# Performance work log

Hardware: AMD Instinct MI355X
Metric: run time of the kernel (lower is better)

## Reference

```python
import jax, jax.numpy as jnp
import numpy as np

ROPE_THETA = 10000.0

def _rope(t):
    # t: (B, S, H, D) -- rotate-half RoPE over last dim
    B, S, H, D = t.shape
    inv_freq = 1.0 / (ROPE_THETA ** (jnp.arange(0, D, 2, dtype=jnp.float32) / D))  # (D/2,)
    ang = jnp.arange(S, dtype=jnp.float32)[:, None] * inv_freq[None, :]            # (S, D/2)
    cos = jnp.concatenate([jnp.cos(ang), jnp.cos(ang)], axis=-1)[None, :, None, :] # (1,S,1,D)
    sin = jnp.concatenate([jnp.sin(ang), jnp.sin(ang)], axis=-1)[None, :, None, :]
    t1, t2 = jnp.split(t, 2, axis=-1)
    rot = jnp.concatenate([-t2, t1], axis=-1)
    return t * cos.astype(t.dtype) + rot * sin.astype(t.dtype)

def setup_inputs() -> dict:
    key = jax.random.key(0)
    kx, kq, kk, kv, ko = jax.random.split(key, 5)
    B, S, DIM = 2, 2048, 2048
    x = jax.random.normal(kx, (B, S, DIM), dtype=jnp.float32)
    mask = jnp.tril(jnp.ones((S, S), dtype=bool))[None, None, :, :]  # causal (1,1,S,S)
    scale = DIM ** -0.5
    wq = jax.random.normal(kq, (DIM, DIM), dtype=jnp.float32) * scale
    wk = jax.random.normal(kk, (DIM, DIM), dtype=jnp.float32) * scale
    wv = jax.random.normal(kv, (DIM, DIM), dtype=jnp.float32) * scale
    wo = jax.random.normal(ko, (DIM, DIM), dtype=jnp.float32) * scale
    return {"x": x, "mask": mask, "wq": wq, "wk": wk, "wv": wv, "wo": wo}

def reference(x, mask, wq, wk, wv, wo):
    B, S, DIM = x.shape
    H = 16
    D = DIM // H
    scale = D ** -0.5
    # nn.Linear: y = x @ W.T
    q = (x @ wq.T).reshape(B, S, H, D)
    k = (x @ wk.T).reshape(B, S, H, D)
    v = (x @ wv.T).reshape(B, S, H, D)
    q = _rope(q)
    k = _rope(k)
    scores = jnp.einsum('bqhd,bkhd->bhqk', q, k) * scale
    scores = jnp.where(mask, scores, -jnp.inf)
    attn = jax.nn.softmax(scores, axis=-1)
    out = jnp.einsum('bhqk,bkhd->bqhd', attn, v).reshape(B, S, DIM)
    return out @ wo.T
```

## Files before the change

### kernel.cpp

```cpp
#include <hip/hip_runtime.h>
#include <cstdint>

typedef unsigned short u16;
typedef uint32_t u32;
typedef __attribute__((ext_vector_type(8))) short bf16x8;
typedef __attribute__((ext_vector_type(4))) float f32x4;
typedef __attribute__((ext_vector_type(16))) float f32x16;

#define DIM_ 2048
#define S_   2048
#define B_   2
#define H_   16
#define HD_  128
#define M_   (B_ * S_)

__device__ __forceinline__ u16 f2b(float f) {
  union { float f; uint32_t u; } v; v.f = f;
  uint32_t u = v.u;
  return (u16)((u + 0x7FFFu + ((u >> 16) & 1u)) >> 16);
}
__device__ __forceinline__ float b2f(u16 h) {
  union { uint32_t u; float f; } v; v.u = ((uint32_t)h) << 16;
  return v.f;
}

__device__ __forceinline__ u32 cvtpk(float lo, float hi) {
  u32 r;
  asm("v_cvt_pk_bf16_f32 %0, %1, %2" : "=v"(r) : "v"(lo), "v"(hi));
  return r;
}

typedef __attribute__((address_space(3))) u16 lds_u16_t;
typedef __attribute__((address_space(1))) const u16 glob_u16_t;

__device__ __forceinline__ void gload16(const u16* g, u16* l) {
  __builtin_amdgcn_global_load_lds((glob_u16_t*)g, (lds_u16_t*)l, 16, 0, 0);
}
#define GLD0(SRC, DST) \
  __builtin_amdgcn_global_load_lds((glob_u16_t*)(SRC), (lds_u16_t*)(DST), 16, 0, 0)

__global__ void convert5_kernel(const float* __restrict__ x, const float* __restrict__ wq,
                                const float* __restrict__ wk, const float* __restrict__ wv,
                                const float* __restrict__ wo, u16* __restrict__ xb,
                                u16* __restrict__ wqb, u16* __restrict__ wkb,
                                u16* __restrict__ wvb, u16* __restrict__ wob) {
  const float* src;
  u16* dst;
  int n;
  switch (blockIdx.y) {
    case 0: src = x;  dst = xb;  n = M_ * DIM_;   break;
    case 1: src = wq; dst = wqb; n = DIM_ * DIM_; break;
    case 2: src = wk; dst = wkb; n = DIM_ * DIM_; break;
    case 3: src = wv; dst = wvb; n = DIM_ * DIM_; break;
    default: src = wo; dst = wob; n = DIM_ * DIM_; break;
  }
  int i = (blockIdx.x * blockDim.x + threadIdx.x) * 4;
  const int stride = gridDim.x * blockDim.x * 4;
  for (; i < n; i += stride) {
    float4 v = *reinterpret_cast<const float4*>(src + i);
    uint64_t p = (uint64_t)f2b(v.x) | ((uint64_t)f2b(v.y) << 16) |
                 ((uint64_t)f2b(v.z) << 32) | ((uint64_t)f2b(v.w) << 48);
    *reinterpret_cast<uint64_t*>(dst + i) = p;
  }
}

__global__ void rope_table_kernel(float* __restrict__ cosT, float* __restrict__ sinT) {
  int i = blockIdx.x * blockDim.x + threadIdx.x;
  if (i >= S_ * 64) return;
  int s = i >> 6, d = i & 63;
  float inv = powf(10000.0f, -(float)d * (1.0f / 64.0f));
  float ang = (float)s * inv;
  cosT[i] = cosf(ang);
  sinT[i] = sinf(ang);
}

#define NT_ 32

#define LDA(DST, BASE)                                                         \
  _Pragma("unroll") for (int mi = 0; mi < 8; ++mi)                             \
      DST[mi] = *(const bf16x8*)((BASE) + mi * 1024);
#define LDB(DST, BASE)                                                         \
  _Pragma("unroll") for (int ni = 0; ni < NF_; ++ni)                           \
      DST[ni] = *(const bf16x8*)((BASE) +                                      \
          (BPERM_ ? (((ni) & 1) * 1024 + ((ni) >> 1) * 4096) : (ni) * 1024));

#define MFMA_KS(AV, BV)                                                        \
  _Pragma("unroll") for (int mi = 0; mi < 8; ++mi)                             \
    _Pragma("unroll") for (int ni = 0; ni < NF_; ++ni)                         \
        acc[mi][ni] = __builtin_amdgcn_mfma_f32_16x16x32_bf16(                 \
            AV[mi], BV[ni], acc[mi][ni], 0, 0, 0);

#define STAGE(BUF, OFFU) do {                                                  \
    _Pragma("unroll") for (int s = 0; s < ASW_; ++s)                           \
      GLD0(sA + goff + (OFFU) + s * (64 * DIM_),                               \
           lds + (BUF) * BUFSZ_ + s * 4096 + w * 512);                         \
    _Pragma("unroll") for (int s = 0; s < BSW_; ++s)                           \
      GLD0(sB + goff + (OFFU) + s * (64 * DIM_),                               \
           lds + (BUF) * BUFSZ_ + 16384 + s * 4096 + w * 512);                 \
  } while (0)

#define VMC_N() do {                                                           \
    if (ASW_ + BSW_ == 8) asm volatile("s_waitcnt vmcnt(8)" ::: "memory");     \
    else                  asm volatile("s_waitcnt vmcnt(6)" ::: "memory");     \
  } while (0)

#define TILE_N(BUF, NBUF, OFFU) do {                                           \
    LDA(a1, pAk1[BUF]); LDB(b1, pBk1[BUF]);                            \
    __builtin_amdgcn_sched_barrier(0);                                         \
    __builtin_amdgcn_s_setprio(1);                                             \
    MFMA_KS(a0, b0);                                                  \
    __builtin_amdgcn_s_setprio(0);                                             \
    asm volatile("s_waitcnt lgkmcnt(0)" ::: "memory");                         \
    __builtin_amdgcn_sched_barrier(0);                                         \
    __builtin_amdgcn_s_barrier();                                      \
    STAGE(BUF, OFFU);                                                          \
    __builtin_amdgcn_sched_barrier(0);                                         \
    VMC_N();                                                                   \
    __builtin_amdgcn_sched_barrier(0);                                         \
    __builtin_amdgcn_s_barrier();                                      \
    LDA(a0, pAk0[NBUF]); LDB(b0, pBk0[NBUF]);                          \
    __builtin_amdgcn_sched_barrier(0);                                         \
    __builtin_amdgcn_s_setprio(1);                                             \
    MFMA_KS(a1, b1);                                                  \
    __builtin_amdgcn_s_setprio(0);                                             \
  } while (0)

#define TILE_P(BUF, NBUF) do {                                   \
    LDA(a1, pAk1[BUF]); LDB(b1, pBk1[BUF]);                                    \
    __builtin_amdgcn_sched_barrier(0);                                         \
    __builtin_amdgcn_s_setprio(1);                                             \
    MFMA_KS(a0, b0);                                                           \
    __builtin_amdgcn_s_setprio(0);                                             \
    asm volatile("s_waitcnt lgkmcnt(0)" ::: "memory");                         \
    __builtin_amdgcn_sched_barrier(0);                                         \
    asm volatile("s_waitcnt vmcnt(0)" ::: "memory");                           \
    __builtin_amdgcn_sched_barrier(0);                                         \
    __builtin_amdgcn_s_barrier();                                              \
    LDA(a0, pAk0[NBUF]); LDB(b0, pBk0[NBUF]);                                  \
    __builtin_amdgcn_sched_barrier(0);                                         \
    __builtin_amdgcn_s_setprio(1);                                             \
    MFMA_KS(a1, b1);                                                           \
    __builtin_amdgcn_s_setprio(0);                                             \
  } while (0)

#define TILE_L(BUF) do {                                         \
    LDA(a1, pAk1[BUF]); LDB(b1, pBk1[BUF]);                                    \
    __builtin_amdgcn_sched_barrier(0);                                         \
    MFMA_KS(a0, b0);                                                           \
    MFMA_KS(a1, b1);                                                           \
  } while (0)

#define GEMM_V2_BODY(BN_, BPERM__)                                             \
  constexpr int NF_ = (BN_) / 64;                                              \
  constexpr int BPERM_ = (BPERM__);                                            \
  constexpr int ASW_ = 4;                                                      \
  constexpr int BSW_ = (BN_) / 64;                                             \
  constexpr int BUFSZ_ = 16384 + (BN_) * 64;                                   \
  const int tid = threadIdx.x;                                                 \
  const int lane = tid & 63;                                                   \
  const int w = tid >> 6;                                                      \
  const int wm = w >> 2, wn = w & 3;                                           \
  const int l15 = lane & 15, lg = lane >> 4;                                   \
  const int goff = (w * 8 + (lane >> 3)) * DIM_ + ((lane & 7) ^ (lane >> 3)) * 8; \
  const int x7 = l15 & 7;                                                      \
  const int lr0 = l15 * 64 + ((lg ^ x7) * 8);                                  \
  const int lr1 = l15 * 64 + (((4 | lg) ^ x7) * 8);                            \
  const int bbase = BPERM_ ? ((wn >> 1) * 8192 + (wn & 1) * 2048)              \
                           : (wn * ((BN_) * 16));                              \
  const u16* pAk0[2] = {lds + wm * 8192 + lr0, lds + BUFSZ_ + wm * 8192 + lr0};\
  const u16* pAk1[2] = {lds + wm * 8192 + lr1, lds + BUFSZ_ + wm * 8192 + lr1};\
  const u16* pBk0[2] = {lds + 16384 + bbase + lr0,                             \
                        lds + BUFSZ_ + 16384 + bbase + lr0};                   \
  const u16* pBk1[2] = {lds + 16384 + bbase + lr1,                             \
                        lds + BUFSZ_ + 16384 + bbase + lr1};                   \
  f32x4 acc[8][NF_];                                                           \
  _Pragma("unroll") for (int i = 0; i < 8; ++i)                                \
    _Pragma("unroll") for (int j = 0; j < NF_; ++j)                            \
        acc[i][j] = (f32x4){0.f, 0.f, 0.f, 0.f};                               \
  bf16x8 a0[8], a1[8], b0[NF_], b1[NF_];                                       \
  STAGE(0, 0);                                                                 \
  STAGE(1, 64);                                                                \
  __builtin_amdgcn_sched_barrier(0);                                           \
  VMC_N();                                                                     \
  __builtin_amdgcn_sched_barrier(0);                                           \
  __builtin_amdgcn_s_barrier();                                                \
  LDA(a0, pAk0[0]); LDB(b0, pBk0[0]);                                          \
  for (int t = 0; t < NT_ - 2; t += 2) {                                       \
    TILE_N(0, 1, 128);                                                         \
    TILE_N(1, 0, 192);                                                         \
    sA += 128; sB += 128;                                                      \
  }                                                                            \
  TILE_P(0, 1);                                                                \
  TILE_L(1);

__global__ __launch_bounds__(512, 2) void gemm256_qkv_kernel(
    const u16* __restrict__ xb, const u16* __restrict__ wqb, const u16* __restrict__ wkb,
    const u16* __restrict__ wvb, u16* __restrict__ qb, u16* __restrict__ kb,
    u16* __restrict__ vb, const float* __restrict__ cosT, const float* __restrict__ sinT) {
  __shared__ __align__(16) u16 lds[65536];

  const int bid = blockIdx.x;
  const int logical = (bid & 7) * 48 + (bid >> 3);
  const int mt = logical / 24;
  const int rem = logical % 24;
  const int z = rem >> 3;
  const int nt = rem & 7;
  const u16* Wm = (z == 0) ? wqb : (z == 1) ? wkb : wvb;
  u16* out = (z == 0) ? qb : (z == 1) ? kb : vb;

  const u16* sA = xb + (size_t)(mt * 256) * DIM_;
  const u16* sB = Wm + (size_t)(nt * 256) * DIM_;

  GEMM_V2_BODY(256, 1)

  const int colbase = nt * 256 + (wn >> 1) * 128 + (wn & 1) * 32;
  if (z < 2) {
#pragma unroll
    for (int mi = 0; mi < 8; ++mi) {
      const int row = mt * 256 + wm * 128 + mi * 16 + lg * 4;
#pragma unroll
      for (int r = 0; r < 4; ++r) {
        const int s = (row + r) & (S_ - 1);
#pragma unroll
        for (int ni = 0; ni < 2; ++ni) {
          const int d = (wn & 1) * 32 + ni * 16 + l15;
          const float c  = cosT[s * 64 + d];
          const float sn = sinT[s * 64 + d];
          const float t1 = acc[mi][ni][r];
          const float t2 = acc[mi][ni + 2][r];
          u16* p = out + (size_t)(row + r) * DIM_ + colbase + ni * 16 + l15;
          p[0]  = f2b(t1 * c - t2 * sn);
          p[64] = f2b(t2 * c + t1 * sn);
        }
      }
    }
  } else {
#pragma unroll
    for (int mi = 0; mi < 8; ++mi)
#pragma unroll
      for (int ni = 0; ni < 4; ++ni) {
        const int row = mt * 256 + wm * 128 + mi * 16 + lg * 4;
        const int col = colbase + (ni & 1) * 16 + (ni >> 1) * 64 + l15;
#pragma unroll
        for (int r = 0; r < 4; ++r)
          out[(size_t)(row + r) * DIM_ + col] = f2b(acc[mi][ni][r]);
      }
  }
}

__global__ __launch_bounds__(512, 2) void gemm_out_v2_kernel(const u16* __restrict__ A,
                                                             const u16* __restrict__ W,
                                                             float* __restrict__ Cf) {
  __shared__ __align__(16) u16 lds[49152];
  const int bid = blockIdx.x;
  const int logical = (bid & 7) * 32 + (bid >> 3);
  const int mt = logical >> 4;
  const int nt = logical & 15;

  const u16* sA = A + (size_t)(mt * 256) * DIM_;
  const u16* sB = W + (size_t)(nt * 128) * DIM_;

  GEMM_V2_BODY(128, 0)

#pragma unroll
  for (int mi = 0; mi < 8; ++mi)
#pragma unroll
    for (int ni = 0; ni < 2; ++ni) {
      const int row = mt * 256 + wm * 128 + mi * 16 + lg * 4;
      const int col = nt * 128 + wn * 32 + ni * 16 + l15;
#pragma unroll
      for (int r = 0; r < 4; ++r)
        Cf[(size_t)(row + r) * DIM_ + col] = acc[mi][ni][r];
    }
}

#define CEXP 0.12751744f

__global__ __launch_bounds__(256, 2) void attn_kernel(const u16* __restrict__ q,
                                                      const u16* __restrict__ k,
                                                      const u16* __restrict__ v,
                                                      u16* __restrict__ ao) {
  __shared__ __align__(16) u16 smem[32768];
  u16* kTl = smem;
  u16* vTl = smem + 16384;

  const int r_    = blockIdx.x;
  const int qt   = 15 - (r_ >> 1);
  const int b    = r_ & 1;
  const int head = blockIdx.y;
  const int t = threadIdx.x;
  const int lane = t & 63;
  const int w = t >> 6;
  const int l31 = lane & 31;
  const int hi = lane >> 5;
  const int kxor = (lane & 7) << 3;
  const int qrow0 = qt * 128 + w * 32;
  const size_t bS = (size_t)b * S_;

  bf16x8 qf[8];
  {
    const u16* qrow = q + (bS + qrow0 + l31) * DIM_ + head * HD_;
#pragma unroll
    for (int st = 0; st < 8; ++st)
      qf[st] = *(const bf16x8*)(qrow + st * 16 + hi * 8);
  }

  f32x16 accO[4];
#pragma unroll
  for (int db = 0; db < 4; ++db)
#pragma unroll
    for (int rr = 0; rr < 16; ++rr) accO[db][rr] = 0.f;
  float m = -1e30f, l = 0.f;

  const int tmax_w = 2 * qt + (w >> 1);
  const int ttend = 2 * qt + 1;

  bf16x8 vv[4];

  auto stageK = [&](int buf, int tt) {
#pragma unroll
    for (int p = 0; p < 4; ++p) {
      const int cid = p * 256 + w * 64 + lane;
      const int kr = cid >> 4;
      const int cg = (cid & 15) ^ (kr & 7);
      gload16(k + (bS + tt * 64 + kr) * DIM_ + head * HD_ + cg * 8,
              kTl + buf * 8192 + (p * 256 + w * 64) * 8);
    }
  };
  auto loadV = [&](int tt) {
#pragma unroll
    for (int p = 0; p < 4; ++p) {
      const int dchunk = p * 4 + w;
      vv[p] = *(const bf16x8*)(v + (bS + tt * 64 + lane) * DIM_ + head * HD_ + dchunk * 8);
    }
  };
  auto writeV = [&](int buf) {
#pragma unroll
    for (int p = 0; p < 4; ++p) {
      const int dchunk = p * 4 + w;
#pragma unroll
      for (int j = 0; j < 8; ++j) {
        const int d = dchunk * 8 + j;
        vTl[buf * 8192 + d * 64 + (lane ^ ((d & 7) << 3))] = (u16)vv[p][j];
      }
    }
  };

  stageK(0, 0);
  loadV(0);
  writeV(0);
  __syncthreads();

  for (int tt = 0; tt <= ttend; ++tt) {
    const int cur = tt & 1;
    const int alt = cur ^ 1;

    if (tt + 1 <= ttend) {
      stageK(alt, tt + 1);
      loadV(tt + 1);
    }

    if (tt <= tmax_w) {
      const u16* kB = kTl + cur * 8192;
      const u16* vB = vTl + cur * 8192;
      f32x16 sA, sB;
#pragma unroll
      for (int rr = 0; rr < 16; ++rr) { sA[rr] = 0.f; sB[rr] = 0.f; }
      __builtin_amdgcn_s_setprio(1);
#pragma unroll
      for (int st = 0; st < 8; ++st) {
        const int dc = st * 16 + hi * 8;
        bf16x8 k0 = *(const bf16x8*)(kB + l31 * 128 + (dc ^ kxor));
        bf16x8 k1 = *(const bf16x8*)(kB + (32 + l31) * 128 + (dc ^ kxor));
        sA = __builtin_amdgcn_mfma_f32_32x32x16_bf16(k0, qf[st], sA, 0, 0, 0);
        sB = __builtin_amdgcn_mfma_f32_32x32x16_bf16(k1, qf[st], sB, 0, 0, 0);
      }
      __builtin_amdgcn_s_setprio(0);

      const int qg = qrow0 + l31;
      if (tt * 64 + 63 > qrow0) {
        const int kb = tt * 64 + 4 * hi;
#pragma unroll
        for (int rr = 0; rr < 16; ++rr) {
          const int kg = kb + (rr & 3) + 8 * (rr >> 2);
          sA[rr] = (kg <= qg) ? sA[rr] : -1e30f;
          sB[rr] = (kg + 32 <= qg) ? sB[rr] : -1e30f;
        }
      }

      float mx[8];
#pragma unroll
      for (int i = 0; i < 8; ++i)
        mx[i] = fmaxf(fmaxf(sA[i], sA[i + 8]), fmaxf(sB[i], sB[i + 8]));
#pragma unroll
      for (int i = 0; i < 4; ++i) mx[i] = fmaxf(mx[i], mx[i + 4]);
      float pm = fmaxf(fmaxf(mx[0], mx[1]), fmaxf(mx[2], mx[3]));
      pm = fmaxf(pm, __shfl_xor(pm, 32));
      const float mN = fmaxf(m, pm);
      if (!__all(pm - m <= 90.5f)) {
        const float osc = exp2f((m - mN) * CEXP);
        l *= osc;
#pragma unroll
        for (int db = 0; db < 4; ++db)
#pragma unroll
          for (int rr = 0; rr < 16; ++rr) accO[db][rr] *= osc;
        m = mN;
      }
      const float mc = m * CEXP;
      float lsv[4] = {0.f, 0.f, 0.f, 0.f};
#pragma unroll
      for (int rr = 0; rr < 16; ++rr) {
        const float pa = exp2f(__builtin_fmaf(sA[rr], CEXP, -mc));
        const float pb = exp2f(__builtin_fmaf(sB[rr], CEXP, -mc));
        sA[rr] = pa; sB[rr] = pb;
        lsv[rr & 3] += pa + pb;
      }
      float ls = (lsv[0] + lsv[1]) + (lsv[2] + lsv[3]);
      ls += __shfl_xor(ls, 32);
      l += ls;

#define PV_STEP(ARR, R0, ST2)                                                      \
      {                                                                            \
        u32 a0 = cvtpk(ARR[(R0) + 0], ARR[(R0) + 1]);                              \
        u32 a1 = cvtpk(ARR[(R0) + 2], ARR[(R0) + 3]);                              \
        u32 b0 = cvtpk(ARR[(R0) + 4], ARR[(R0) + 5]);                              \
        u32 b1 = cvtpk(ARR[(R0) + 6], ARR[(R0) + 7]);                              \
        asm("v_permlane32_swap_b32 %0, %1" : "+v"(a0), "+v"(b0));                  \
        asm("v_permlane32_swap_b32 %0, %1" : "+v"(a1), "+v"(b1));                  \
        union { u32 uu[4]; bf16x8 v8; } pf;                                        \
        pf.uu[0] = a0; pf.uu[1] = a1; pf.uu[2] = b0; pf.uu[3] = b1;                \
        const int ko = (ST2) * 16 + hi * 8;                                        \
        __builtin_amdgcn_s_setprio(1);                                             \
        _Pragma("unroll")                                                          \
        for (int db = 0; db < 4; ++db) {                                           \
          const int dr = db * 32 + l31;                                            \
          bf16x8 vf = *(const bf16x8*)(vB + dr * 64 + (ko ^ kxor));                \
          accO[db] =                                                               \
              __builtin_amdgcn_mfma_f32_32x32x16_bf16(vf, pf.v8, accO[db], 0, 0, 0); \
        }                                                                          \
        __builtin_amdgcn_s_setprio(0);                                             \
      }
      PV_STEP(sA, 0, 0)
      PV_STEP(sA, 8, 1)
      PV_STEP(sB, 0, 2)
      PV_STEP(sB, 8, 3)
#undef PV_STEP
    }

    if (tt + 1 <= ttend) writeV(alt);
    __syncthreads();
  }

  const float linv = 1.0f / l;
  u16* oT = smem + w * 4352;
#pragma unroll
  for (int db = 0; db < 4; ++db)
#pragma unroll
    for (int q4 = 0; q4 < 4; ++q4) {
      const int dbase = db * 32 + q4 * 8 + hi * 4;
      const u32 lo = cvtpk(accO[db][q4 * 4 + 0] * linv, accO[db][q4 * 4 + 1] * linv);
      const u32 hiw = cvtpk(accO[db][q4 * 4 + 2] * linv, accO[db][q4 * 4 + 3] * linv);
      *(u32*)(oT + l31 * 136 + dbase) = lo;
      *(u32*)(oT + l31 * 136 + dbase + 2) = hiw;
    }
  __syncthreads();
#pragma unroll
  for (int i = 0; i < 8; ++i) {
    const int cid = i * 64 + lane;
    const int qloc = cid >> 4;
    const int c = cid & 15;
    const bf16x8 val = *(const bf16x8*)(oT + qloc * 136 + c * 8);
    *(bf16x8*)(ao + (bS + qrow0 + qloc) * DIM_ + head * HD_ + c * 8) = val;
  }
}

extern "C" void kernel_launch(void* const* d_in, const int* in_sizes, int n_in,
                              void* d_out, int out_size, void* d_ws, size_t ws_size,
                              hipStream_t stream) {
  const float* x  = (const float*)d_in[0];
  const float* wq = (const float*)d_in[2];
  const float* wk = (const float*)d_in[3];
  const float* wv = (const float*)d_in[4];
  const float* wo = (const float*)d_in[5];

  char* ws = (char*)d_ws;
  size_t off = 0;
  auto carve = [&](size_t bytes) { char* p = ws + off; off += bytes; return p; };
  u16* xb   = (u16*)carve((size_t)M_ * DIM_ * 2);
  u16* wqb  = (u16*)carve((size_t)DIM_ * DIM_ * 2);
  u16* wkb  = (u16*)carve((size_t)DIM_ * DIM_ * 2);
  u16* wvb  = (u16*)carve((size_t)DIM_ * DIM_ * 2);
  u16* wob  = (u16*)carve((size_t)DIM_ * DIM_ * 2);
  u16* qb   = (u16*)carve((size_t)M_ * DIM_ * 2);
  u16* kb   = (u16*)carve((size_t)M_ * DIM_ * 2);
  u16* vb   = (u16*)carve((size_t)M_ * DIM_ * 2);
  u16* aob  = (u16*)carve((size_t)M_ * DIM_ * 2);
  float* cosT = (float*)carve((size_t)S_ * 64 * 4);
  float* sinT = (float*)carve((size_t)S_ * 64 * 4);
  if (off > ws_size) return;

  dim3 gc(1024, 5);
  convert5_kernel<<<gc, 256, 0, stream>>>(x, wq, wk, wv, wo, xb, wqb, wkb, wvb, wob);
  rope_table_kernel<<<512, 256, 0, stream>>>(cosT, sinT);

  gemm256_qkv_kernel<<<384, 512, 0, stream>>>(xb, wqb, wkb, wvb, qb, kb, vb, cosT, sinT);

  dim3 ga(32, H_);
  attn_kernel<<<ga, 256, 0, stream>>>(qb, kb, vb, aob);

  gemm_out_v2_kernel<<<256, 512, 0, stream>>>(aob, wob, (float*)d_out);
}
```

Measured before the change: 280.8 us.

## Transpose RoPE tables for float4 loads and remap attention grid by batch

The cos/sin tables are now stored dimension-major (d*S + s), so the QKV GEMM epilogue can fetch four consecutive sequence positions with one float4 load instead of four scalar loads per element. Separately, the attention grid moves from a flat 32-wide x dimension to (16, H, B), and batch 1 walks query tiles in the reverse order of batch 0. The aim is to cut epilogue load traffic and to change how the causal long and short tiles are scheduled and balanced. The epilogue change depends on row being a multiple of 4 for the float4 alignment.

```diff
diff --git a/kernel.cpp b/kernel.cpp
--- a/kernel.cpp
+++ b/kernel.cpp
@@ -66,8 +66,9 @@
 
 __global__ void rope_table_kernel(float* __restrict__ cosT, float* __restrict__ sinT) {
   int i = blockIdx.x * blockDim.x + threadIdx.x;
-  if (i >= S_ * 64) return;
-  int s = i >> 6, d = i & 63;
+  if (i >= 64 * S_) return;
+  int d = i >> 11;
+  int s = i & (S_ - 1);
   float inv = powf(10000.0f, -(float)d * (1.0f / 64.0f));
   float ang = (float)s * inv;
   cosT[i] = cosf(ang);
@@ -218,19 +219,21 @@
 #pragma unroll
     for (int mi = 0; mi < 8; ++mi) {
       const int row = mt * 256 + wm * 128 + mi * 16 + lg * 4;
-#pragma unroll
-      for (int r = 0; r < 4; ++r) {
-        const int s = (row + r) & (S_ - 1);
-#pragma unroll
-        for (int ni = 0; ni < 2; ++ni) {
-          const int d = (wn & 1) * 32 + ni * 16 + l15;
-          const float c  = cosT[s * 64 + d];
-          const float sn = sinT[s * 64 + d];
+      const int s = row & (S_ - 1);
+#pragma unroll
+      for (int ni = 0; ni < 2; ++ni) {
+        const int d = (wn & 1) * 32 + ni * 16 + l15;
+        const float4 c4 = *(const float4*)(cosT + d * S_ + s);
+        const float4 s4 = *(const float4*)(sinT + d * S_ + s);
+        const float cc[4]  = {c4.x, c4.y, c4.z, c4.w};
+        const float ssn[4] = {s4.x, s4.y, s4.z, s4.w};
+        u16* p = out + (size_t)row * DIM_ + colbase + ni * 16 + l15;
+#pragma unroll
+        for (int r = 0; r < 4; ++r) {
           const float t1 = acc[mi][ni][r];
           const float t2 = acc[mi][ni + 2][r];
-          u16* p = out + (size_t)(row + r) * DIM_ + colbase + ni * 16 + l15;
-          p[0]  = f2b(t1 * c - t2 * sn);
-          p[64] = f2b(t2 * c + t1 * sn);
+          p[(size_t)r * DIM_]      = f2b(t1 * cc[r] - t2 * ssn[r]);
+          p[(size_t)r * DIM_ + 64] = f2b(t2 * cc[r] + t1 * ssn[r]);
         }
       }
     }
@@ -284,10 +287,9 @@
   u16* kTl = smem;
   u16* vTl = smem + 16384;
 
-  const int r_    = blockIdx.x;
-  const int qt   = 15 - (r_ >> 1);
-  const int b    = r_ & 1;
+  const int qt   = blockIdx.z ? (int)blockIdx.x : (int)(gridDim.x - 1 - blockIdx.x);
   const int head = blockIdx.y;
+  const int b    = blockIdx.z;
   const int t = threadIdx.x;
   const int lane = t & 63;
   const int w = t >> 6;
@@ -495,8 +497,8 @@
   u16* kb   = (u16*)carve((size_t)M_ * DIM_ * 2);
   u16* vb   = (u16*)carve((size_t)M_ * DIM_ * 2);
   u16* aob  = (u16*)carve((size_t)M_ * DIM_ * 2);
-  float* cosT = (float*)carve((size_t)S_ * 64 * 4);
-  float* sinT = (float*)carve((size_t)S_ * 64 * 4);
+  float* cosT = (float*)carve((size_t)64 * S_ * 4);
+  float* sinT = (float*)carve((size_t)64 * S_ * 4);
   if (off > ws_size) return;
 
   dim3 gc(1024, 5);
@@ -505,7 +507,7 @@
 
   gemm256_qkv_kernel<<<384, 512, 0, stream>>>(xb, wqb, wkb, wvb, qb, kb, vb, cosT, sinT);
 
-  dim3 ga(32, H_);
+  dim3 ga(16, H_, B_);
   attn_kernel<<<ga, 256, 0, stream>>>(qb, kb, vb, aob);
 
   gemm_out_v2_kernel<<<256, 512, 0, stream>>>(aob, wob, (float*)d_out);
```

New measurement: 272.6 us. -2.9%, faster.
